# Kernel tuning notes

Measured on AMD Instinct MI355X. Metric: run time of the kernel, lower is better.

## Reference

```python
import jax, jax.numpy as jnp
import numpy as np

N = 16384        # tokens (batch*seq)
D_MODEL = 4096
D_HALF = D_MODEL // 2
NUM_EXPERTS = 64
TOP_K = 4
SCALE = 2.0


def setup_inputs() -> dict:
    key = jax.random.key(0)
    k_u, k_ex, k_ey = jax.random.split(key, 3)
    u = jax.random.normal(k_u, (N, D_MODEL), dtype=jnp.float32)
    E_x = jax.random.normal(k_ex, (D_HALF, NUM_EXPERTS), dtype=jnp.float32) * 0.01
    E_y = jax.random.normal(k_ey, (D_HALF, NUM_EXPERTS), dtype=jnp.float32) * 0.01
    bias = jnp.zeros((NUM_EXPERTS,), dtype=jnp.float32)
    # torus-shape scalar parameters (torch init values)
    c = jnp.float32(2.0)
    d = jnp.float32(2.0)
    a1 = jnp.float32(4.0)
    b1 = jnp.float32(4.0)
    return {"u": u, "E_x": E_x, "E_y": E_y, "bias": bias,
            "c": c, "d": d, "a1": a1, "b1": b1, "top_k": TOP_K}


def reference(u, E_x, E_y, bias, c, d, a1, b1, top_k):
    d_half = E_x.shape[0]
    num_experts = E_x.shape[1]
    # dual small GEMM + tanh squash onto [-scale, scale]
    x = jnp.tanh(u[..., :d_half] @ E_x) * SCALE        # [N, E]
    y = jnp.tanh(u[..., d_half:] @ E_y) * SCALE        # [N, E]
    xa, ya = jnp.abs(x), jnp.abs(y)
    # 4CM torus: f(x,y) = (|x|^a1 + |y|^b1) * exp(-(|x|^c + |y|^d))
    scores = (xa ** a1 + ya ** b1) * jnp.exp(-(xa ** c + ya ** d)) + bias
    topk_s, topk_i = jax.lax.top_k(scores, top_k)       # [N, k]
    probs = jax.nn.softmax(scores, axis=-1)             # [N, E]
    aux_loss = jnp.sum(jnp.mean(probs, axis=0) ** 2) * num_experts
    return topk_i, topk_s, scores, aux_loss
```

## Files before the change

kernel.cpp:

```cpp
#include <hip/hip_runtime.h>
#include <math.h>

#define N_TOK 16384
#define DM    4096
#define DH    2048
#define NE    64
#define TBK   64
#define TOPK  4
#define KQ    1024
#define NSTEP 32

#define OFF_TI  0
#define OFF_TS  (N_TOK * TOPK)
#define OFF_SC  (N_TOK * TOPK * 2)
#define OFF_AUX (N_TOK * TOPK * 2 + N_TOK * NE)

typedef __attribute__((ext_vector_type(4)))  float  f32x4;
typedef __attribute__((ext_vector_type(16))) float  f32x16;
typedef __attribute__((ext_vector_type(8)))  __bf16 bf16x8;

#define BSPLIT_ELEMS (2 * 64 * 3 * 2 * 2 * 64 * 8)

__device__ __forceinline__ void split3(float a, __bf16& h, __bf16& m, __bf16& l) {
    h = (__bf16)a;
    float r = a - (float)h;
    m = (__bf16)r;
    float r2 = r - (float)m;
    l = (__bf16)r2;
}

__global__ __launch_bounds__(256) void prep_B(
    const float* __restrict__ Ex, const float* __restrict__ Ey,
    __bf16* __restrict__ Bws)
{
    const int t    = blockIdx.x * 256 + threadIdx.x;
    const int lane = t & 63;
    const int sk   = (t >> 6) & 1;
    const int et   = (t >> 7) & 1;
    const int ks   = (t >> 8) & 63;
    const int h    = (t >> 14) & 1;
    const float* E = h ? Ey : Ex;
    const int e  = et * 32 + (lane & 31);
    const int k0 = ks * 32 + sk * 16 + (lane >> 5) * 8;
    bf16x8 vh, vm, vl;
    #pragma unroll
    for (int j = 0; j < 8; ++j) {
        __bf16 hh, mm, ll;
        split3(E[(size_t)(k0 + j) * NE + e], hh, mm, ll);
        vh[j] = hh; vm[j] = mm; vl[j] = ll;
    }
    #pragma unroll
    for (int s = 0; s < 3; ++s) {
        size_t base = ((((((size_t)h * 64 + ks) * 3 + s) * 2 + et) * 2 + sk) * 64 + lane) * 8;
        *(bf16x8*)(Bws + base) = (s == 0) ? vh : (s == 1) ? vm : vl;
    }
}

__global__ __launch_bounds__(512, 2) void torus_mfma(
    const float* __restrict__ u, const __bf16* __restrict__ Bws,
    const float* __restrict__ bias,
    const float* __restrict__ cp, const float* __restrict__ dp,
    const float* __restrict__ a1p, const float* __restrict__ b1p,
    float* __restrict__ out, float* __restrict__ esum)
{
    __shared__ float pre[2][NE][68];
    __shared__ float stile[TBK][NE + 1];
    __shared__ float s_m[TBK], s_inv[TBK];

    const int tid  = threadIdx.x;
    const int t0   = blockIdx.x * TBK;
    const int lane = tid & 63;
    const int wv   = tid >> 6;
    const int h    = wv >> 2;
    const int kh   = (wv >> 1) & 1;
    const int th   = wv & 1;
    const int lr   = lane & 31;
    const int lkh  = lane >> 5;

    const float* ap = u + (size_t)(t0 + th * 32 + lr) * DM + h * DH + kh * KQ + lkh * 8;
    const __bf16* bp0 = Bws + ((size_t)h * 64 + kh * 32) * 6144 + lane * 8;

    f32x16 acc[2][2] = {};
    f32x4  rA[2][4];

    auto load_raw = [&](f32x4 (&r)[4], int s) {
        const float* p = ap + s * 32;
        r[0] = *(const f32x4*)(p);
        r[1] = *(const f32x4*)(p + 4);
        r[2] = *(const f32x4*)(p + 16);
        r[3] = *(const f32x4*)(p + 20);
    };

    auto step = [&](int s, f32x4 (&r)[4]) {
        const __bf16* bp = bp0 + (size_t)s * 6144;
        bf16x8 bh[2][2], bm[2][2], bl[2][2];
        #pragma unroll
        for (int et = 0; et < 2; ++et)
            #pragma unroll
            for (int sk = 0; sk < 2; ++sk) {
                bh[et][sk] = *(const bf16x8*)(bp + (0 * 4 + et * 2 + sk) * 512);
                bm[et][sk] = *(const bf16x8*)(bp + (1 * 4 + et * 2 + sk) * 512);
                bl[et][sk] = *(const bf16x8*)(bp + (2 * 4 + et * 2 + sk) * 512);
            }
        __builtin_amdgcn_sched_barrier(0);
        bf16x8 sh[2], sm[2], sl[2];
        #pragma unroll
        for (int sk = 0; sk < 2; ++sk)
            #pragma unroll
            for (int q = 0; q < 2; ++q)
                #pragma unroll
                for (int j = 0; j < 4; ++j) {
                    __bf16 hh, mm, ll;
                    split3(r[sk * 2 + q][j], hh, mm, ll);
                    sh[sk][q * 4 + j] = hh; sm[sk][q * 4 + j] = mm; sl[sk][q * 4 + j] = ll;
                }
        const int sp = (s + 2 < NSTEP) ? s + 2 : s;
        load_raw(r, sp);
        __builtin_amdgcn_sched_barrier(0);
        #pragma unroll
        for (int et = 0; et < 2; ++et)
            #pragma unroll
            for (int sk = 0; sk < 2; ++sk) {
                acc[sk][et] = __builtin_amdgcn_mfma_f32_32x32x16_bf16(sh[sk], bh[et][sk], acc[sk][et], 0, 0, 0);
                acc[sk][et] = __builtin_amdgcn_mfma_f32_32x32x16_bf16(sm[sk], bh[et][sk], acc[sk][et], 0, 0, 0);
                acc[sk][et] = __builtin_amdgcn_mfma_f32_32x32x16_bf16(sl[sk], bh[et][sk], acc[sk][et], 0, 0, 0);
            }
        #pragma unroll
        for (int et = 0; et < 2; ++et)
            #pragma unroll
            for (int sk = 0; sk < 2; ++sk) {
                acc[sk][et] = __builtin_amdgcn_mfma_f32_32x32x16_bf16(sh[sk], bm[et][sk], acc[sk][et], 0, 0, 0);
                acc[sk][et] = __builtin_amdgcn_mfma_f32_32x32x16_bf16(sm[sk], bm[et][sk], acc[sk][et], 0, 0, 0);
            }
        #pragma unroll
        for (int et = 0; et < 2; ++et)
            #pragma unroll
            for (int sk = 0; sk < 2; ++sk)
                acc[sk][et] = __builtin_amdgcn_mfma_f32_32x32x16_bf16(sh[sk], bl[et][sk], acc[sk][et], 0, 0, 0);
        __builtin_amdgcn_sched_barrier(0);
    };

    load_raw(rA[0], 0);
    load_raw(rA[1], 1);
    #pragma unroll 1
    for (int s = 0; s < NSTEP; s += 2) {
        step(s,     rA[0]);
        step(s + 1, rA[1]);
    }

    __syncthreads();
    if (kh == 0) {
        #pragma unroll
        for (int et = 0; et < 2; ++et) {
            f32x16 a = acc[0][et] + acc[1][et];
            #pragma unroll
            for (int q = 0; q < 4; ++q) {
                int e  = et * 32 + lr;
                int tk = th * 32 + q * 8 + 4 * lkh;
                f32x4 v = { a[q*4+0], a[q*4+1], a[q*4+2], a[q*4+3] };
                *(f32x4*)&pre[h][e][tk] = v;
            }
        }
    }
    __syncthreads();
    if (kh == 1) {
        #pragma unroll
        for (int et = 0; et < 2; ++et) {
            f32x16 a = acc[0][et] + acc[1][et];
            #pragma unroll
            for (int q = 0; q < 4; ++q) {
                int e  = et * 32 + lr;
                int tk = th * 32 + q * 8 + 4 * lkh;
                f32x4 v = { a[q*4+0], a[q*4+1], a[q*4+2], a[q*4+3] };
                f32x4 o = *(f32x4*)&pre[h][e][tk];
                v += o;
                *(f32x4*)&pre[h][e][tk] = v;
            }
        }
    }
    __syncthreads();

    {
        const float c_ = *cp, d_ = *dp, a1_ = *a1p, b1_ = *b1p;
        const int tk = tid & 63;
        const int e0 = (tid >> 6) * 8;
        #pragma unroll
        for (int i = 0; i < 8; ++i) {
            int e = e0 + i;
            float x = pre[0][e][tk];
            float y = pre[1][e][tk];
            x = tanhf(x) * 2.0f; y = tanhf(y) * 2.0f;
            float xa = fabsf(x), ya = fabsf(y);
            float sc = (powf(xa, a1_) + powf(ya, b1_)) *
                       expf(-(powf(xa, c_) + powf(ya, d_))) + bias[e];
            stile[tk][e] = sc;
        }
    }
    __syncthreads();

    if (tid < TBK) {
        const int t = tid;
        float bv[TOPK]; int bi[TOPK];
        #pragma unroll
        for (int p = 0; p < TOPK; ++p) {
            float best = -INFINITY; int besti = 0;
            for (int e = 0; e < NE; ++e) {
                float v = stile[t][e];
                bool taken = false;
                #pragma unroll
                for (int q = 0; q < p; ++q) taken = taken || (bi[q] == e);
                if (!taken && v > best) { best = v; besti = e; }
            }
            bv[p] = best; bi[p] = besti;
        }
        const float m = bv[0];
        float denom = 0.0f;
        for (int e = 0; e < NE; ++e) denom += expf(stile[t][e] - m);
        const float inv = 1.0f / denom;
        s_m[t] = m; s_inv[t] = inv;
        #pragma unroll
        for (int p = 0; p < TOPK; ++p) {
            out[OFF_TI + (size_t)(t0 + t) * TOPK + p] = (float)bi[p];
            out[OFF_TS + (size_t)(t0 + t) * TOPK + p] = bv[p];
        }
    }
    __syncthreads();

    if (tid < NE) {
        const int e = tid;
        float cs = 0.0f;
        for (int t = 0; t < TBK; ++t)
            cs += expf(stile[t][e] - s_m[t]) * s_inv[t];
        atomicAdd(&esum[e], cs);
    }

    for (int idx = tid; idx < TBK * NE; idx += 512)
        out[OFF_SC + (size_t)t0 * NE + idx] = stile[idx >> 6][idx & (NE - 1)];
}

__global__ __launch_bounds__(64) void torus_aux(const float* __restrict__ esum,
                                                float* __restrict__ out)
{
    const int e = threadIdx.x;
    float s = esum[e] * (1.0f / (float)N_TOK);
    float v = s * s;
    #pragma unroll
    for (int off = 32; off > 0; off >>= 1) v += __shfl_down(v, off);
    if (e == 0) out[OFF_AUX] = v * (float)NE;
}

extern "C" void kernel_launch(void* const* d_in, const int* in_sizes, int n_in,
                              void* d_out, int out_size, void* d_ws, size_t ws_size,
                              hipStream_t stream) {
    const float* u    = (const float*)d_in[0];
    const float* Ex   = (const float*)d_in[1];
    const float* Ey   = (const float*)d_in[2];
    const float* bias = (const float*)d_in[3];
    const float* cp   = (const float*)d_in[4];
    const float* dp   = (const float*)d_in[5];
    const float* a1p  = (const float*)d_in[6];
    const float* b1p  = (const float*)d_in[7];
    float* out = (float*)d_out;
    __bf16* Bws = (__bf16*)d_ws;
    float* esum = (float*)((char*)d_ws + (size_t)BSPLIT_ELEMS * sizeof(__bf16));

    prep_B<<<128, 256, 0, stream>>>(Ex, Ey, Bws);
    hipMemsetAsync(esum, 0, NE * sizeof(float), stream);
    torus_mfma<<<N_TOK / TBK, 512, 0, stream>>>(u, Bws, bias, cp, dp, a1p, b1p, out, esum);
    torus_aux<<<1, 64, 0, stream>>>(esum, out);
}
```

Measured before the change: 124.0 us.

## Stage u tiles via async global_load_lds ring buffer with smaller token blocks

Replaces register-prefetched u loads with direct global-to-LDS async loads into a 4-deep per-wave swizzled ring buffer. B fragments are now double-buffered in registers one step ahead. The block tile shrinks from 64 to 32 tokens and from 512 to 256 threads, which doubles the grid. The bf16 split now uses bit masking (truncation) instead of rounding conversions. This aims to hide global memory latency and cut VALU cost, at the price of a hand-tuned vmcnt wait, 64KB of LDS per block, and slightly different split numerics.

After: 109.2 us. -11.9%, faster.

```diff
diff --git a/kernel.cpp b/kernel.cpp
--- a/kernel.cpp
+++ b/kernel.cpp
@@ -1,11 +1,12 @@
 #include <hip/hip_runtime.h>
 #include <math.h>
+#include <stdint.h>
 
 #define N_TOK 16384
 #define DM    4096
 #define DH    2048
 #define NE    64
-#define TBK   64
+#define TBK   32
 #define TOPK  4
 #define KQ    1024
 #define NSTEP 32
@@ -18,6 +19,7 @@
 typedef __attribute__((ext_vector_type(4)))  float  f32x4;
 typedef __attribute__((ext_vector_type(16))) float  f32x16;
 typedef __attribute__((ext_vector_type(8)))  __bf16 bf16x8;
+typedef __attribute__((ext_vector_type(8)))  unsigned short u16x8;
 
 #define BSPLIT_ELEMS (2 * 64 * 3 * 2 * 2 * 64 * 8)
 
@@ -27,6 +29,13 @@
     m = (__bf16)r;
     float r2 = r - (float)m;
     l = (__bf16)r2;
+}
+
+__device__ __forceinline__ void stage16(const float* g, void* l) {
+    __builtin_amdgcn_global_load_lds(
+        (const __attribute__((address_space(1))) unsigned int*)(uintptr_t)g,
+        (__attribute__((address_space(3))) unsigned int*)(uintptr_t)l,
+        16, 0, 0);
 }
 
 __global__ __launch_bounds__(256) void prep_B(
@@ -56,99 +65,146 @@
     }
 }
 
-__global__ __launch_bounds__(512, 2) void torus_mfma(
+__global__ __launch_bounds__(256, 2) void torus_mfma(
     const float* __restrict__ u, const __bf16* __restrict__ Bws,
     const float* __restrict__ bias,
     const float* __restrict__ cp, const float* __restrict__ dp,
     const float* __restrict__ a1p, const float* __restrict__ b1p,
     float* __restrict__ out, float* __restrict__ esum)
 {
-    __shared__ float pre[2][NE][68];
-    __shared__ float stile[TBK][NE + 1];
-    __shared__ float s_m[TBK], s_inv[TBK];
+    __shared__ __align__(16) unsigned char smem[65536];
 
     const int tid  = threadIdx.x;
     const int t0   = blockIdx.x * TBK;
     const int lane = tid & 63;
     const int wv   = tid >> 6;
-    const int h    = wv >> 2;
-    const int kh   = (wv >> 1) & 1;
-    const int th   = wv & 1;
+    const int h    = wv >> 1;
+    const int kh   = wv & 1;
     const int lr   = lane & 31;
     const int lkh  = lane >> 5;
 
-    const float* ap = u + (size_t)(t0 + th * 32 + lr) * DM + h * DH + kh * KQ + lkh * 8;
+    float* ring = (float*)(smem + wv * 16384);
+
+    const int   srow  = lane >> 3;
+    const int   schk  = (lane & 7) ^ srow;
+    const float* gbase = u + (size_t)(t0 + srow) * DM + h * DH + kh * KQ + schk * 4;
+
+    auto stage = [&](int s) {
+        const float* g = gbase + s * 32;
+        unsigned char* lb = (unsigned char*)ring + (s & 3) * 4096;
+        #pragma unroll
+        for (int i = 0; i < 4; ++i)
+            stage16(g + (size_t)i * 8 * DM, lb + i * 1024);
+    };
+
+    int rb[4];
+    {
+        const int ch0 = 2 * lkh, ch1 = 2 * lkh + 1, ch2 = 4 + 2 * lkh, ch3 = 5 + 2 * lkh;
+        rb[0] = lr * 32 + ((ch0 ^ (lr & 7)) * 4);
+        rb[1] = lr * 32 + ((ch1 ^ (lr & 7)) * 4);
+        rb[2] = lr * 32 + ((ch2 ^ (lr & 7)) * 4);
+        rb[3] = lr * 32 + ((ch3 ^ (lr & 7)) * 4);
+    }
+
     const __bf16* bp0 = Bws + ((size_t)h * 64 + kh * 32) * 6144 + lane * 8;
+    auto loadB = [&](bf16x8 (&b)[12], int s) {
+        const __bf16* bp = bp0 + (size_t)s * 6144;
+        #pragma unroll
+        for (int et = 0; et < 2; ++et)
+            #pragma unroll
+            for (int sk = 0; sk < 2; ++sk) {
+                b[0 + et * 2 + sk] = *(const bf16x8*)(bp + (0 + et * 2 + sk) * 512);
+                b[4 + et * 2 + sk] = *(const bf16x8*)(bp + (4 + et * 2 + sk) * 512);
+                b[8 + et * 2 + sk] = *(const bf16x8*)(bp + (8 + et * 2 + sk) * 512);
+            }
+    };
 
     f32x16 acc[2][2] = {};
-    f32x4  rA[2][4];
-
-    auto load_raw = [&](f32x4 (&r)[4], int s) {
-        const float* p = ap + s * 32;
-        r[0] = *(const f32x4*)(p);
-        r[1] = *(const f32x4*)(p + 4);
-        r[2] = *(const f32x4*)(p + 16);
-        r[3] = *(const f32x4*)(p + 20);
-    };
-
-    auto step = [&](int s, f32x4 (&r)[4]) {
-        const __bf16* bp = bp0 + (size_t)s * 6144;
-        bf16x8 bh[2][2], bm[2][2], bl[2][2];
+
+    auto body = [&](int s, bf16x8 (&bu)[12], bf16x8 (&bn)[12]) {
+        const int sn = (s + 1 < NSTEP) ? s + 1 : s;
+        loadB(bn, sn);
+        if (s + 3 < NSTEP) stage(s + 3);
+        __builtin_amdgcn_sched_barrier(0);
+        asm volatile("s_waitcnt vmcnt(36)" ::: "memory");
+        __builtin_amdgcn_sched_barrier(0);
+        const float* rp = ring + (s & 3) * 1024;
+        f32x4 r0 = *(const f32x4*)(rp + rb[0]);
+        f32x4 r1 = *(const f32x4*)(rp + rb[1]);
+        f32x4 r2 = *(const f32x4*)(rp + rb[2]);
+        f32x4 r3 = *(const f32x4*)(rp + rb[3]);
+        u16x8 sh[2], sm[2], sl[2];
+        #pragma unroll
+        for (int q = 0; q < 2; ++q)
+            #pragma unroll
+            for (int j = 0; j < 4; ++j) {
+                {
+                    float a = (q == 0 ? r0 : r1)[j];
+                    unsigned h32 = __float_as_uint(a) & 0xFFFF0000u;
+                    float rr = a - __uint_as_float(h32);
+                    unsigned m32 = __float_as_uint(rr) & 0xFFFF0000u;
+                    float r2f = rr - __uint_as_float(m32);
+                    sh[0][q * 4 + j] = (unsigned short)(h32 >> 16);
+                    sm[0][q * 4 + j] = (unsigned short)(m32 >> 16);
+                    sl[0][q * 4 + j] = (unsigned short)(__float_as_uint(r2f) >> 16);
+                }
+                {
+                    float a = (q == 0 ? r2 : r3)[j];
+                    unsigned h32 = __float_as_uint(a) & 0xFFFF0000u;
+                    float rr = a - __uint_as_float(h32);
+                    unsigned m32 = __float_as_uint(rr) & 0xFFFF0000u;
+                    float r2f = rr - __uint_as_float(m32);
+                    sh[1][q * 4 + j] = (unsigned short)(h32 >> 16);
+                    sm[1][q * 4 + j] = (unsigned short)(m32 >> 16);
+                    sl[1][q * 4 + j] = (unsigned short)(__float_as_uint(r2f) >> 16);
+                }
+            }
+        __builtin_amdgcn_sched_barrier(0);
         #pragma unroll
         for (int et = 0; et < 2; ++et)
             #pragma unroll
             for (int sk = 0; sk < 2; ++sk) {
-                bh[et][sk] = *(const bf16x8*)(bp + (0 * 4 + et * 2 + sk) * 512);
-                bm[et][sk] = *(const bf16x8*)(bp + (1 * 4 + et * 2 + sk) * 512);
-                bl[et][sk] = *(const bf16x8*)(bp + (2 * 4 + et * 2 + sk) * 512);
-            }
-        __builtin_amdgcn_sched_barrier(0);
-        bf16x8 sh[2], sm[2], sl[2];
-        #pragma unroll
-        for (int sk = 0; sk < 2; ++sk)
-            #pragma unroll
-            for (int q = 0; q < 2; ++q)
-                #pragma unroll
-                for (int j = 0; j < 4; ++j) {
-                    __bf16 hh, mm, ll;
-                    split3(r[sk * 2 + q][j], hh, mm, ll);
-                    sh[sk][q * 4 + j] = hh; sm[sk][q * 4 + j] = mm; sl[sk][q * 4 + j] = ll;
-                }
-        const int sp = (s + 2 < NSTEP) ? s + 2 : s;
-        load_raw(r, sp);
-        __builtin_amdgcn_sched_barrier(0);
+                bf16x8 vh_ = __builtin_bit_cast(bf16x8, sh[sk]);
+                bf16x8 vm_ = __builtin_bit_cast(bf16x8, sm[sk]);
+                bf16x8 vl_ = __builtin_bit_cast(bf16x8, sl[sk]);
+                acc[sk][et] = __builtin_amdgcn_mfma_f32_32x32x16_bf16(vh_, bu[0 + et * 2 + sk], acc[sk][et], 0, 0, 0);
+                acc[sk][et] = __builtin_amdgcn_mfma_f32_32x32x16_bf16(vm_, bu[0 + et * 2 + sk], acc[sk][et], 0, 0, 0);
+                acc[sk][et] = __builtin_amdgcn_mfma_f32_32x32x16_bf16(vl_, bu[0 + et * 2 + sk], acc[sk][et], 0, 0, 0);
+            }
         #pragma unroll
         for (int et = 0; et < 2; ++et)
             #pragma unroll
             for (int sk = 0; sk < 2; ++sk) {
-                acc[sk][et] = __builtin_amdgcn_mfma_f32_32x32x16_bf16(sh[sk], bh[et][sk], acc[sk][et], 0, 0, 0);
-                acc[sk][et] = __builtin_amdgcn_mfma_f32_32x32x16_bf16(sm[sk], bh[et][sk], acc[sk][et], 0, 0, 0);
-                acc[sk][et] = __builtin_amdgcn_mfma_f32_32x32x16_bf16(sl[sk], bh[et][sk], acc[sk][et], 0, 0, 0);
+                bf16x8 vh_ = __builtin_bit_cast(bf16x8, sh[sk]);
+                bf16x8 vm_ = __builtin_bit_cast(bf16x8, sm[sk]);
+                acc[sk][et] = __builtin_amdgcn_mfma_f32_32x32x16_bf16(vh_, bu[4 + et * 2 + sk], acc[sk][et], 0, 0, 0);
+                acc[sk][et] = __builtin_amdgcn_mfma_f32_32x32x16_bf16(vm_, bu[4 + et * 2 + sk], acc[sk][et], 0, 0, 0);
             }
         #pragma unroll
         for (int et = 0; et < 2; ++et)
             #pragma unroll
             for (int sk = 0; sk < 2; ++sk) {
-                acc[sk][et] = __builtin_amdgcn_mfma_f32_32x32x16_bf16(sh[sk], bm[et][sk], acc[sk][et], 0, 0, 0);
-                acc[sk][et] = __builtin_amdgcn_mfma_f32_32x32x16_bf16(sm[sk], bm[et][sk], acc[sk][et], 0, 0, 0);
-            }
-        #pragma unroll
-        for (int et = 0; et < 2; ++et)
-            #pragma unroll
-            for (int sk = 0; sk < 2; ++sk)
-                acc[sk][et] = __builtin_amdgcn_mfma_f32_32x32x16_bf16(sh[sk], bl[et][sk], acc[sk][et], 0, 0, 0);
+                bf16x8 vh_ = __builtin_bit_cast(bf16x8, sh[sk]);
+                acc[sk][et] = __builtin_amdgcn_mfma_f32_32x32x16_bf16(vh_, bu[8 + et * 2 + sk], acc[sk][et], 0, 0, 0);
+            }
         __builtin_amdgcn_sched_barrier(0);
     };
 
-    load_raw(rA[0], 0);
-    load_raw(rA[1], 1);
+    stage(0); stage(1); stage(2);
+    bf16x8 b0[12], b1[12];
+    loadB(b0, 0);
     #pragma unroll 1
     for (int s = 0; s < NSTEP; s += 2) {
-        step(s,     rA[0]);
-        step(s + 1, rA[1]);
-    }
-
-    __syncthreads();
+        body(s,     b0, b1);
+        body(s + 1, b1, b0);
+    }
+
+    __syncthreads();
+    float (*pre)[NE][36]   = (float(*)[NE][36])smem;
+    float (*stile)[NE + 1] = (float(*)[NE + 1])(smem + 18432);
+    float* s_m  = (float*)(smem + 18432 + 8320);
+    float* s_inv = s_m + TBK;
+
     if (kh == 0) {
         #pragma unroll
         for (int et = 0; et < 2; ++et) {
@@ -156,7 +212,7 @@
             #pragma unroll
             for (int q = 0; q < 4; ++q) {
                 int e  = et * 32 + lr;
-                int tk = th * 32 + q * 8 + 4 * lkh;
+                int tk = q * 8 + 4 * lkh;
                 f32x4 v = { a[q*4+0], a[q*4+1], a[q*4+2], a[q*4+3] };
                 *(f32x4*)&pre[h][e][tk] = v;
             }
@@ -170,7 +226,7 @@
             #pragma unroll
             for (int q = 0; q < 4; ++q) {
                 int e  = et * 32 + lr;
-                int tk = th * 32 + q * 8 + 4 * lkh;
+                int tk = q * 8 + 4 * lkh;
                 f32x4 v = { a[q*4+0], a[q*4+1], a[q*4+2], a[q*4+3] };
                 f32x4 o = *(f32x4*)&pre[h][e][tk];
                 v += o;
@@ -182,8 +238,8 @@
 
     {
         const float c_ = *cp, d_ = *dp, a1_ = *a1p, b1_ = *b1p;
-        const int tk = tid & 63;
-        const int e0 = (tid >> 6) * 8;
+        const int tk = tid & 31;
+        const int e0 = (tid >> 5) * 8;
         #pragma unroll
         for (int i = 0; i < 8; ++i) {
             int e = e0 + i;
@@ -234,7 +290,7 @@
         atomicAdd(&esum[e], cs);
     }
 
-    for (int idx = tid; idx < TBK * NE; idx += 512)
+    for (int idx = tid; idx < TBK * NE; idx += 256)
         out[OFF_SC + (size_t)t0 * NE + idx] = stile[idx >> 6][idx & (NE - 1)];
 }
 
@@ -266,6 +322,6 @@
 
     prep_B<<<128, 256, 0, stream>>>(Ex, Ey, Bws);
     hipMemsetAsync(esum, 0, NE * sizeof(float), stream);
-    torus_mfma<<<N_TOK / TBK, 512, 0, stream>>>(u, Bws, bias, cp, dp, a1p, b1p, out, esum);
+    torus_mfma<<<N_TOK / TBK, 256, 0, stream>>>(u, Bws, bias, cp, dp, a1p, b1p, out, esum);
     torus_aux<<<1, 64, 0, stream>>>(esum, out);
 }
```
